# Kernel optimization log

Measured on AMD Instinct MI355X. Metric: run time of the kernel, lower is better.

## Reference

```python
import jax, jax.numpy as jnp
import numpy as np

K = 3          # kernel_size (local window)
PAD = 1        # padding = (K-1)//2 -> 'same' output size
GROUPS = 8
C_OUT = 64


def _unfold3d(x, k):
    """x: [B,C,Dp,Hp,Wp] -> [B,C,D,H,W,kd,kh,kw] sliding windows (stride 1)."""
    B, C, Dp, Hp, Wp = x.shape
    D, H, W = Dp - k + 1, Hp - k + 1, Wp - k + 1
    idx_d = jnp.arange(D)[:, None] + jnp.arange(k)[None, :]
    idx_h = jnp.arange(H)[:, None] + jnp.arange(k)[None, :]
    idx_w = jnp.arange(W)[:, None] + jnp.arange(k)[None, :]
    x = x[:, :, idx_d]              # [B,C,D,kd,Hp,Wp]
    x = x[:, :, :, :, idx_h]        # [B,C,D,kd,H,kh,Wp]
    x = x[:, :, :, :, :, :, idx_w]  # [B,C,D,kd,H,kh,W,kw]
    return jnp.transpose(x, (0, 1, 2, 4, 6, 3, 5, 7))


def setup_inputs() -> dict:
    key = jax.random.key(0)
    ks = jax.random.split(key, 7)
    B, Cin, D, H, W = 1, 64, 16, 64, 64
    c3 = C_OUT // 3                 # 21
    rest = C_OUT - 2 * c3           # 22
    fan_out_scale = np.sqrt(2.0 / C_OUT)  # kaiming_normal fan_out, relu
    x = jax.random.normal(ks[0], (B, Cin, D, H, W), dtype=jnp.float32)
    w_q = jax.random.normal(ks[1], (C_OUT, Cin), dtype=jnp.float32) * fan_out_scale
    w_k = jax.random.normal(ks[2], (C_OUT, Cin), dtype=jnp.float32) * fan_out_scale
    w_v = jax.random.normal(ks[3], (C_OUT, Cin), dtype=jnp.float32) * fan_out_scale
    rel_d = jax.random.normal(ks[4], (c3, 1, 1, 1, K, 1, 1), dtype=jnp.float32)
    rel_h = jax.random.normal(ks[5], (c3, 1, 1, 1, 1, K, 1), dtype=jnp.float32)
    rel_w = jax.random.normal(ks[6], (rest, 1, 1, 1, 1, 1, K), dtype=jnp.float32)
    return {"x": x, "w_q": w_q, "w_k": w_k, "w_v": w_v,
            "rel_d": rel_d, "rel_h": rel_h, "rel_w": rel_w}


def reference(x, w_q, w_k, w_v, rel_d, rel_h, rel_w):
    B, Cin, D, H, W = x.shape
    cg = C_OUT // GROUPS
    c3 = C_OUT // 3
    # 1x1x1 convs (bias=False): plain channel mixing. conv(pad(x)) == pad(conv(x)).
    q = jnp.einsum('oc,bcdhw->bodhw', w_q, x)
    k = jnp.einsum('oc,bcdhw->bodhw', w_k, x)
    v = jnp.einsum('oc,bcdhw->bodhw', w_v, x)
    pad = [(0, 0), (0, 0), (PAD, PAD), (PAD, PAD), (PAD, PAD)]
    k = jnp.pad(k, pad)
    v = jnp.pad(v, pad)
    k_win = _unfold3d(k, K)   # [B,Co,D,H,W,kd,kh,kw]
    v_win = _unfold3d(v, K)
    # split relative position bias across channel thirds
    k_win = jnp.concatenate([
        k_win[:, :c3] + rel_d,
        k_win[:, c3:2 * c3] + rel_h,
        k_win[:, 2 * c3:] + rel_w,
    ], axis=1)
    Kv = K * K * K
    k_win = k_win.reshape(B, GROUPS, cg, D, H, W, Kv)
    v_win = v_win.reshape(B, GROUPS, cg, D, H, W, Kv)
    qg = q.reshape(B, GROUPS, cg, D, H, W, 1)
    attn = jax.nn.softmax(qg * k_win, axis=-1)
    out = jnp.einsum('bncdhwk,bncdhwk->bncdhw', attn, v_win)
    return out.reshape(B, C_OUT, D, H, W)
```

## Files before the change

kernel.cpp:

```cpp
#include <hip/hip_runtime.h>

#define SP    65536
#define DD    16
#define HH    64
#define WW    64
#define CIN   64
#define COUT  64

#define RP    68

#define LOG2E 1.44269504f


typedef __attribute__((ext_vector_type(8))) short bf16x8;
typedef __attribute__((ext_vector_type(4))) float f32x4;

__device__ __forceinline__ unsigned short f2bf(float f) {
    const unsigned u = __float_as_uint(f);
    return (unsigned short)((u + 0x7FFFu + ((u >> 16) & 1u)) >> 16);
}
__device__ __forceinline__ float bf2f(unsigned short h) {
    return __uint_as_float((unsigned)h << 16);
}

__global__ __launch_bounds__(256) void proj(const float* __restrict__ x,
                                            const float* __restrict__ wq,
                                            const float* __restrict__ wk,
                                            const float* __restrict__ wv,
                                            float* __restrict__ q,
                                            float* __restrict__ k,
                                            float* __restrict__ v) {
    __shared__ __align__(16) unsigned short xh [64][72];
    __shared__ __align__(16) unsigned short xlo[64][72];
    __shared__ __align__(16) unsigned short wh [64][72];
    __shared__ __align__(16) unsigned short wlo[64][72];

    const int t  = threadIdx.x;
    const int p0 = blockIdx.x * 64;
    const int m  = blockIdx.y;

    const float* __restrict__ wsel = (m == 0) ? wq : (m == 1) ? wk : wv;
    float* __restrict__       osel = (m == 0) ? q  : (m == 1) ? k  : v;

#pragma unroll
    for (int i = 0; i < 2; ++i) {
        const int f  = t + 256 * i;
        const int c2 = (f >> 4) * 2;
        const int jj = f & 15;
        const float4 a = *(const float4*)(x + c2 * SP + p0 + jj * 4);
        const float4 b = *(const float4*)(x + (c2 + 1) * SP + p0 + jj * 4);
        const float* af = (const float*)&a;
        const float* bf = (const float*)&b;
#pragma unroll
        for (int e = 0; e < 4; ++e) {
            const int j = jj * 4 + e;
            const unsigned short ah = f2bf(af[e]);
            const unsigned short bh = f2bf(bf[e]);
            const unsigned short al = f2bf(af[e] - bf2f(ah));
            const unsigned short bl = f2bf(bf[e] - bf2f(bh));
            *(unsigned*)&xh [j][c2] = (unsigned)ah | ((unsigned)bh << 16);
            *(unsigned*)&xlo[j][c2] = (unsigned)al | ((unsigned)bl << 16);
        }
    }
#pragma unroll
    for (int i = 0; i < 4; ++i) {
        const int f  = t + 256 * i;
        const int o  = f >> 4;
        const int jj = f & 15;
        const float4 w4 = *(const float4*)(wsel + o * CIN + jj * 4);
        const float* wf = (const float*)&w4;
        unsigned short h0 = f2bf(wf[0]), h1 = f2bf(wf[1]);
        unsigned short h2 = f2bf(wf[2]), h3 = f2bf(wf[3]);
        unsigned short l0 = f2bf(wf[0] - bf2f(h0)), l1 = f2bf(wf[1] - bf2f(h1));
        unsigned short l2 = f2bf(wf[2] - bf2f(h2)), l3 = f2bf(wf[3] - bf2f(h3));
        *(uint2*)&wh [o][jj * 4] = make_uint2((unsigned)h0 | ((unsigned)h1 << 16),
                                              (unsigned)h2 | ((unsigned)h3 << 16));
        *(uint2*)&wlo[o][jj * 4] = make_uint2((unsigned)l0 | ((unsigned)l1 << 16),
                                              (unsigned)l2 | ((unsigned)l3 << 16));
    }
    __syncthreads();

    const int lane  = t & 63;
    const int wid   = t >> 6;
    const int lo16  = lane & 15;
    const int lg    = lane >> 4;
    const int otile = wid * 16;

    const bf16x8 Ah0 = *(const bf16x8*)&wh [otile + lo16][lg * 8];
    const bf16x8 Ah1 = *(const bf16x8*)&wh [otile + lo16][32 + lg * 8];
    const bf16x8 Al0 = *(const bf16x8*)&wlo[otile + lo16][lg * 8];
    const bf16x8 Al1 = *(const bf16x8*)&wlo[otile + lo16][32 + lg * 8];

    const float scale = (m == 0) ? LOG2E : 1.f;

#pragma unroll
    for (int jt = 0; jt < 4; ++jt) {
        const int jr = jt * 16 + lo16;
        const bf16x8 Bh0 = *(const bf16x8*)&xh [jr][lg * 8];
        const bf16x8 Bl0 = *(const bf16x8*)&xlo[jr][lg * 8];
        const bf16x8 Bh1 = *(const bf16x8*)&xh [jr][32 + lg * 8];
        const bf16x8 Bl1 = *(const bf16x8*)&xlo[jr][32 + lg * 8];
        f32x4 hh = {0.f, 0.f, 0.f, 0.f};
        f32x4 hl = {0.f, 0.f, 0.f, 0.f};
        f32x4 lh = {0.f, 0.f, 0.f, 0.f};
        hh = __builtin_amdgcn_mfma_f32_16x16x32_bf16(Ah0, Bh0, hh, 0, 0, 0);
        hl = __builtin_amdgcn_mfma_f32_16x16x32_bf16(Ah0, Bl0, hl, 0, 0, 0);
        lh = __builtin_amdgcn_mfma_f32_16x16x32_bf16(Al0, Bh0, lh, 0, 0, 0);
        hh = __builtin_amdgcn_mfma_f32_16x16x32_bf16(Ah1, Bh1, hh, 0, 0, 0);
        hl = __builtin_amdgcn_mfma_f32_16x16x32_bf16(Ah1, Bl1, hl, 0, 0, 0);
        lh = __builtin_amdgcn_mfma_f32_16x16x32_bf16(Al1, Bh1, lh, 0, 0, 0);
        float* op = osel + (otile + lg * 4) * SP + p0 + jt * 16 + lo16;
#pragma unroll
        for (int r = 0; r < 4; ++r)
            op[r * SP] = (hh[r] + hl[r] + lh[r]) * scale;
    }
}

__device__ __forceinline__ float dpp_shr1(float x) {
    return __int_as_float(__builtin_amdgcn_mov_dpp(__float_as_int(x), 0x111, 0xf, 0xf, true));
}
__device__ __forceinline__ float dpp_shl1(float x) {
    return __int_as_float(__builtin_amdgcn_mov_dpp(__float_as_int(x), 0x101, 0xf, 0xf, true));
}

template<int AXIS>
__device__ __forceinline__ void attn_walk(const float* __restrict__ kt,
                                          const float* __restrict__ vt,
                                          const float (&ql)[4],
                                          float r0, float r1, float r2,
                                          int wg, int hl, int dl,
                                          float (&s)[4], float (&a)[4]) {
#pragma unroll
    for (int kd = 0; kd < 3; ++kd) {
        const float rdd = (kd == 0) ? r0 : (kd == 1) ? r1 : r2;
#pragma unroll
        for (int kh = 0; kh < 3; ++kh) {
            const float rkh = (kh == 0) ? r0 : (kh == 1) ? r1 : r2;
            const float rr  = (AXIS == 0) ? rdd : (AXIS == 1) ? rkh : 0.f;
            const int off = ((dl + kd) * 6 + hl + kh) * RP + wg * 4;
            const float4 km = *(const float4*)(kt + off);
            const float4 vm = *(const float4*)(vt + off);
            const float kl = dpp_shr1(km.w), kr = dpp_shl1(km.x);
            const float vl = dpp_shr1(vm.w), vr = dpp_shl1(vm.x);
            const float krow[6] = { kl, km.x, km.y, km.z, km.w, kr };
            const float vrow[6] = { vl, vm.x, vm.y, vm.z, vm.w, vr };
#pragma unroll
            for (int wi = 0; wi < 4; ++wi) {
                const float qv = ql[wi];
#pragma unroll
                for (int kw = 0; kw < 3; ++kw) {
                    const float rc = (AXIS == 2)
                                   ? ((kw == 0) ? r0 : (kw == 1) ? r1 : r2)
                                   : rr;
                    const float e = __builtin_amdgcn_exp2f(qv * (krow[wi + kw] + rc));
                    s[wi] += e;
                    a[wi] = fmaf(e, vrow[wi + kw], a[wi]);
                }
            }
        }
    }
}

__global__ __launch_bounds__(256) void attn(const float* __restrict__ kbuf,
                                            const float* __restrict__ vbuf,
                                            const float* __restrict__ qbuf,
                                            const float* __restrict__ rel_d,
                                            const float* __restrict__ rel_h,
                                            const float* __restrict__ rel_w,
                                            float* __restrict__ out) {
    __shared__ float kt[36 * RP];
    __shared__ float vt[36 * RP];

    const int dt = blockIdx.x;
    const int ht = blockIdx.y;
    const int o  = blockIdx.z;

    const int d0 = dt * 4;
    const int h0 = ht * 4;
    const int t  = threadIdx.x;

    const float* __restrict__ kc = kbuf + o * SP;
    const float* __restrict__ vc = vbuf + o * SP;

#pragma unroll
    for (int i = 0; i < 5; ++i) {
        const int idx = t + 256 * i;
        if (idx < 1152) {
            const bool isv = idx >= 576;
            const int rem  = isv ? idx - 576 : idx;
            const int row  = rem >> 4;
            const int j    = rem & 15;
            const int nd   = row / 6;
            const int nh   = row - nd * 6;
            const int dpg  = d0 - 1 + nd;
            const int hpg  = h0 - 1 + nh;
            float4 val = make_float4(0.f, 0.f, 0.f, 0.f);
            if ((unsigned)dpg < (unsigned)DD && (unsigned)hpg < (unsigned)HH) {
                const float* src = (isv ? vc : kc) + (dpg * HH + hpg) * WW + j * 4;
                val = *(const float4*)src;
            }
            *(float4*)((isv ? vt : kt) + row * RP + j * 4) = val;
        }
    }

    const int wg = t & 15;
    const int hl = (t >> 4) & 3;
    const int dl = t >> 6;

    const int dabs = d0 + dl;
    const int habs = h0 + hl;

    float ql[4];
    {
        const float4 q4 = *(const float4*)(qbuf + o * SP + (dabs * HH + habs) * WW + wg * 4);
        ql[0] = q4.x; ql[1] = q4.y;
        ql[2] = q4.z; ql[3] = q4.w;
    }

    __syncthreads();

    float s[4] = {};
    float a[4] = {};

    if (o < 21) {
        attn_walk<0>(kt, vt, ql, rel_d[o * 3], rel_d[o * 3 + 1], rel_d[o * 3 + 2],
                     wg, hl, dl, s, a);
    } else if (o < 42) {
        const int b = o - 21;
        attn_walk<1>(kt, vt, ql, rel_h[b * 3], rel_h[b * 3 + 1], rel_h[b * 3 + 2],
                     wg, hl, dl, s, a);
    } else {
        const int b = o - 42;
        attn_walk<2>(kt, vt, ql, rel_w[b * 3], rel_w[b * 3 + 1], rel_w[b * 3 + 2],
                     wg, hl, dl, s, a);
    }

    float4 ov;
    ov.x = a[0] * __builtin_amdgcn_rcpf(s[0]);
    ov.y = a[1] * __builtin_amdgcn_rcpf(s[1]);
    ov.z = a[2] * __builtin_amdgcn_rcpf(s[2]);
    ov.w = a[3] * __builtin_amdgcn_rcpf(s[3]);
    *(float4*)(out + o * SP + (dabs * HH + habs) * WW + wg * 4) = ov;
}

extern "C" void kernel_launch(void* const* d_in, const int* in_sizes, int n_in,
                              void* d_out, int out_size, void* d_ws, size_t ws_size,
                              hipStream_t stream) {
    const float* x     = (const float*)d_in[0];
    const float* w_q   = (const float*)d_in[1];
    const float* w_k   = (const float*)d_in[2];
    const float* w_v   = (const float*)d_in[3];
    const float* rel_d = (const float*)d_in[4];
    const float* rel_h = (const float*)d_in[5];
    const float* rel_w = (const float*)d_in[6];
    float* out = (float*)d_out;

    float* ws = (float*)d_ws;
    float* q  = ws;
    float* k  = ws + (size_t)COUT * SP;
    float* v  = ws + 2 * (size_t)COUT * SP;

    proj<<<dim3(SP / 64, 3), 256, 0, stream>>>(x, w_q, w_k, w_v, q, k, v);
    attn<<<dim3(4, 16, 64), 256, 0, stream>>>(k, v, q, rel_d, rel_h, rel_w, out);
}
```

Measured before the change: 118.9 us.

## Drop LDS staging in attention kernel and read K/V halo directly from global

The attention kernel no longer stages the 6x6 row halo of K and V into shared memory behind a barrier. Each thread now loads its float4 rows straight from global memory, relying on L1/L2 for reuse, and masks out-of-range rows. It also folds the d/h relative bias into the K row once instead of once per exp, and stops unrolling the kd loop. This removes the cooperative copy, the LDS traffic and the __syncthreads, at the cost of redundant global and cache loads and a less unrolled inner loop.

```diff
diff --git a/kernel.cpp b/kernel.cpp
--- a/kernel.cpp
+++ b/kernel.cpp
@@ -6,8 +6,6 @@
 #define WW    64
 #define CIN   64
 #define COUT  64
-
-#define RP    68
 
 #define LOG2E 1.44269504f
 
@@ -124,35 +122,47 @@
 }
 
 template<int AXIS>
-__device__ __forceinline__ void attn_walk(const float* __restrict__ kt,
-                                          const float* __restrict__ vt,
+__device__ __forceinline__ void attn_walk(const float* __restrict__ kc,
+                                          const float* __restrict__ vc,
                                           const float (&ql)[4],
                                           float r0, float r1, float r2,
-                                          int wg, int hl, int dl,
+                                          int wg, int dabs, int habs,
                                           float (&s)[4], float (&a)[4]) {
-#pragma unroll
+#pragma unroll 1
     for (int kd = 0; kd < 3; ++kd) {
         const float rdd = (kd == 0) ? r0 : (kd == 1) ? r1 : r2;
+        const int dpg   = dabs - 1 + kd;
+        const bool okd  = (unsigned)dpg < (unsigned)DD;
 #pragma unroll
         for (int kh = 0; kh < 3; ++kh) {
             const float rkh = (kh == 0) ? r0 : (kh == 1) ? r1 : r2;
-            const float rr  = (AXIS == 0) ? rdd : (AXIS == 1) ? rkh : 0.f;
-            const int off = ((dl + kd) * 6 + hl + kh) * RP + wg * 4;
-            const float4 km = *(const float4*)(kt + off);
-            const float4 vm = *(const float4*)(vt + off);
+            const float rr  = (AXIS == 0) ? rdd : rkh;
+            const int hpg   = habs - 1 + kh;
+            const bool ok   = okd && ((unsigned)hpg < (unsigned)HH);
+            const int off   = ok ? ((dpg * HH + hpg) * WW + wg * 4) : 0;
+            float4 km = *(const float4*)(kc + off);
+            float4 vm = *(const float4*)(vc + off);
+            if (!ok) {
+                km = make_float4(0.f, 0.f, 0.f, 0.f);
+                vm = make_float4(0.f, 0.f, 0.f, 0.f);
+            }
             const float kl = dpp_shr1(km.w), kr = dpp_shl1(km.x);
             const float vl = dpp_shr1(vm.w), vr = dpp_shl1(vm.x);
-            const float krow[6] = { kl, km.x, km.y, km.z, km.w, kr };
+            float krow[6] = { kl, km.x, km.y, km.z, km.w, kr };
             const float vrow[6] = { vl, vm.x, vm.y, vm.z, vm.w, vr };
+            if (AXIS != 2) {
+#pragma unroll
+                for (int j = 0; j < 6; ++j) krow[j] += rr;
+            }
 #pragma unroll
             for (int wi = 0; wi < 4; ++wi) {
                 const float qv = ql[wi];
 #pragma unroll
                 for (int kw = 0; kw < 3; ++kw) {
-                    const float rc = (AXIS == 2)
-                                   ? ((kw == 0) ? r0 : (kw == 1) ? r1 : r2)
-                                   : rr;
-                    const float e = __builtin_amdgcn_exp2f(qv * (krow[wi + kw] + rc));
+                    const float arg = (AXIS == 2)
+                                    ? (krow[wi + kw] + ((kw == 0) ? r0 : (kw == 1) ? r1 : r2))
+                                    : krow[wi + kw];
+                    const float e = __builtin_amdgcn_exp2f(qv * arg);
                     s[wi] += e;
                     a[wi] = fmaf(e, vrow[wi + kw], a[wi]);
                 }
@@ -168,9 +178,6 @@
                                             const float* __restrict__ rel_h,
                                             const float* __restrict__ rel_w,
                                             float* __restrict__ out) {
-    __shared__ float kt[36 * RP];
-    __shared__ float vt[36 * RP];
-
     const int dt = blockIdx.x;
     const int ht = blockIdx.y;
     const int o  = blockIdx.z;
@@ -181,27 +188,6 @@
 
     const float* __restrict__ kc = kbuf + o * SP;
     const float* __restrict__ vc = vbuf + o * SP;
-
-#pragma unroll
-    for (int i = 0; i < 5; ++i) {
-        const int idx = t + 256 * i;
-        if (idx < 1152) {
-            const bool isv = idx >= 576;
-            const int rem  = isv ? idx - 576 : idx;
-            const int row  = rem >> 4;
-            const int j    = rem & 15;
-            const int nd   = row / 6;
-            const int nh   = row - nd * 6;
-            const int dpg  = d0 - 1 + nd;
-            const int hpg  = h0 - 1 + nh;
-            float4 val = make_float4(0.f, 0.f, 0.f, 0.f);
-            if ((unsigned)dpg < (unsigned)DD && (unsigned)hpg < (unsigned)HH) {
-                const float* src = (isv ? vc : kc) + (dpg * HH + hpg) * WW + j * 4;
-                val = *(const float4*)src;
-            }
-            *(float4*)((isv ? vt : kt) + row * RP + j * 4) = val;
-        }
-    }
 
     const int wg = t & 15;
     const int hl = (t >> 4) & 3;
@@ -217,22 +203,20 @@
         ql[2] = q4.z; ql[3] = q4.w;
     }
 
-    __syncthreads();
-
     float s[4] = {};
     float a[4] = {};
 
     if (o < 21) {
-        attn_walk<0>(kt, vt, ql, rel_d[o * 3], rel_d[o * 3 + 1], rel_d[o * 3 + 2],
-                     wg, hl, dl, s, a);
+        attn_walk<0>(kc, vc, ql, rel_d[o * 3], rel_d[o * 3 + 1], rel_d[o * 3 + 2],
+                     wg, dabs, habs, s, a);
     } else if (o < 42) {
         const int b = o - 21;
-        attn_walk<1>(kt, vt, ql, rel_h[b * 3], rel_h[b * 3 + 1], rel_h[b * 3 + 2],
-                     wg, hl, dl, s, a);
+        attn_walk<1>(kc, vc, ql, rel_h[b * 3], rel_h[b * 3 + 1], rel_h[b * 3 + 2],
+                     wg, dabs, habs, s, a);
     } else {
         const int b = o - 42;
-        attn_walk<2>(kt, vt, ql, rel_w[b * 3], rel_w[b * 3 + 1], rel_w[b * 3 + 2],
-                     wg, hl, dl, s, a);
+        attn_walk<2>(kc, vc, ql, rel_w[b * 3], rel_w[b * 3 + 1], rel_w[b * 3 + 2],
+                     wg, dabs, habs, s, a);
     }
 
     float4 ov;
```

Measured after the change: 115.7 us. 2.7% less time.
